# Optimization experiments

Measured on AMD Instinct MI355X. Metric: run time of the kernel, lower is better.

The kernel has to match this reference:

```python
import jax, jax.numpy as jnp
import numpy as np

N = 60000      # nodes
E = 240000     # edges
H = 256        # hidden_channels
M = 64         # middle_channels
F1 = 12        # num_radial * num_spherical**2
F2 = 6         # num_radial * num_spherical
L = 4          # num_layers (InterBlocks)
NL = 3         # num_output_layers (residual linears per block)
G = 2000       # number of graphs in batch
EPS = 1e-5


def setup_inputs() -> dict:
    key = jax.random.key(0)
    ks = iter(jax.random.split(key, 64))
    def nrm(shape, scale=0.05):
        return jax.random.normal(next(ks), shape, jnp.float32) * scale
    inp = {
        'x_idx': jax.random.randint(next(ks), (N, 9), 0, 178, jnp.int32),
        'edge_attr_idx': jax.random.randint(next(ks), (E, 3), 0, 18, jnp.int32),
        'edge_index': jax.random.randint(next(ks), (2, E), 0, N, jnp.int32),
        'batch': jnp.sort(jax.random.randint(next(ks), (N,), 0, G, jnp.int32)),
        'feature1': jax.random.uniform(next(ks), (E, F1), jnp.float32),
        'feature2': jax.random.uniform(next(ks), (E, F2), jnp.float32),
        # embeddings
        'x_tab': nrm((178, H)), 'e_tab': nrm((18, H)),
        # lin_x: Linear + BN + ReLU
        'linx_w': nrm((L, H, H)), 'linx_b': jnp.zeros((L, H)), 'linx_g': jnp.ones((L, H)), 'linx_be': jnp.zeros((L, H)),
        # lin_feat1: Linear(F1,M) + BN(M) + ReLU + Linear(M,H) + ReLU
        'f1_w1': nrm((L, F1, M)), 'f1_b1': jnp.zeros((L, M)), 'f1_g': jnp.ones((L, M)), 'f1_be': jnp.zeros((L, M)),
        'f1_w2': nrm((L, M, H)), 'f1_b2': jnp.zeros((L, H)),
        # lin_feat2: Linear(F2,M) + BN(M) + ReLU + Linear(M,H) + ReLU
        'f2_w1': nrm((L, F2, M)), 'f2_b1': jnp.zeros((L, M)), 'f2_g': jnp.ones((L, M)), 'f2_be': jnp.zeros((L, M)),
        'f2_w2': nrm((L, M, H)), 'f2_b2': jnp.zeros((L, H)),
        # EdgeGraphConv 1 & 2 (PyG GraphConv: lin_rel(aggr) + lin_root(x), root has no bias)
        'c1_rel_w': nrm((L, H, H)), 'c1_rel_b': jnp.zeros((L, H)), 'c1_root_w': nrm((L, H, H)),
        'c2_rel_w': nrm((L, H, H)), 'c2_rel_b': jnp.zeros((L, H)), 'c2_root_w': nrm((L, H, H)),
        # lin_cat
        'cat_w': nrm((L, 2 * H, H)), 'cat_b': jnp.zeros((L, H)),
        # residual linears
        'lins_w': nrm((L, NL, H, H)), 'lins_b': jnp.zeros((L, NL, H)),
        # GraphNorm
        'gn_w': jnp.ones((L, H)), 'gn_b': jnp.zeros((L, H)), 'gn_ms': jnp.ones((L, H)),
        # final
        'fin_w': nrm((L, H, H)), 'fin_b': jnp.zeros((L, H)),
    }
    return inp


def _bn(h, g, b):
    m = h.mean(0)
    v = jnp.mean((h - m) ** 2, axis=0)
    return (h - m) * jax.lax.rsqrt(v + EPS) * g + b


def _conv(x, src, dst, ew, rel_w, rel_b, root_w):
    # EdgeGraphConv: message = x_j * edge_weight, sum-aggregate at dst
    msg = x[src] * ew                                   # [E, H]
    agg = jax.ops.segment_sum(msg, dst, num_segments=N)  # [N, H]
    return agg @ rel_w + rel_b + x @ root_w


def _graphnorm(h, batch, w, b, ms):
    cnt = jnp.maximum(jax.ops.segment_sum(jnp.ones((h.shape[0], 1), h.dtype), batch, num_segments=G), 1.0)
    mean = jax.ops.segment_sum(h, batch, num_segments=G) / cnt
    out = h - ms * mean[batch]
    var = jax.ops.segment_sum(out ** 2, batch, num_segments=G) / cnt
    return out * jax.lax.rsqrt(var[batch] + EPS) * w + b


def reference(x_idx, edge_attr_idx, edge_index, batch, feature1, feature2, x_tab, e_tab,
              linx_w, linx_b, linx_g, linx_be,
              f1_w1, f1_b1, f1_g, f1_be, f1_w2, f1_b2,
              f2_w1, f2_b1, f2_g, f2_be, f2_w2, f2_b2,
              c1_rel_w, c1_rel_b, c1_root_w, c2_rel_w, c2_rel_b, c2_root_w,
              cat_w, cat_b, lins_w, lins_b, gn_w, gn_b, gn_ms, fin_w, fin_b):
    relu = jax.nn.relu
    x = x_tab[x_idx].sum(1)                 # [N, H] atom-feature embedding sum
    _e = e_tab[edge_attr_idx].sum(1)        # edge embedding (computed, unused downstream as in source)
    src, dst = edge_index[0], edge_index[1]
    for l in range(L):
        xl = relu(_bn(x @ linx_w[l] + linx_b[l], linx_g[l], linx_be[l]))
        w1 = relu(relu(_bn(feature1 @ f1_w1[l] + f1_b1[l], f1_g[l], f1_be[l])) @ f1_w2[l] + f1_b2[l])
        w2 = relu(relu(_bn(feature2 @ f2_w1[l] + f2_b1[l], f2_g[l], f2_be[l])) @ f2_w2[l] + f2_b2[l])
        h1 = relu(_conv(xl, src, dst, w1, c1_rel_w[l], c1_rel_b[l], c1_root_w[l]))
        h2 = relu(_conv(xl, src, dst, w2, c2_rel_w[l], c2_rel_b[l], c2_root_w[l]))
        h = relu(jnp.concatenate([h1, h2], axis=1) @ cat_w[l] + cat_b[l])
        h = h + xl
        for k in range(NL):
            h = relu(h @ lins_w[l, k] + lins_b[l, k]) + h
        h = _graphnorm(h, batch, gn_w[l], gn_b[l], gn_ms[l])
        x = h @ fin_w[l] + fin_b[l]
    return x
```

## Files before the change

### kernel.cpp

```cpp
#include <hip/hip_runtime.h>
#include <cstdint>

constexpr int Nn = 60000;
constexpr int Ee = 240000;
constexpr int Hh = 256;
constexpr int Mm = 64;
constexpr int F1c = 12;
constexpr int Lc = 4;
constexpr int NLc = 3;
constexpr int Gc = 2000;
constexpr float EPSc = 1e-5f;
constexpr int NB = (Nn + 255) / 256;
constexpr int CSB = 256;

typedef _Float16 f16x8 __attribute__((ext_vector_type(8)));
typedef __attribute__((ext_vector_type(4))) float f32x4;
typedef __attribute__((ext_vector_type(4))) unsigned short u16x4;
typedef unsigned short ushortt;

__device__ __forceinline__ ushortt f2h(float f) {
    union { _Float16 h; ushortt u; } c; c.h = (_Float16)f; return c.u;
}
__device__ __forceinline__ float h2f(ushortt u) {
    union { _Float16 h; ushortt u; } c; c.u = u; return (float)c.h;
}

__global__ void embed_x_kernel(const int* __restrict__ xidx, const float* __restrict__ xtab,
                               ushortt* __restrict__ x) {
    int n = blockIdx.x;
    int c = threadIdx.x;
    __shared__ int idx[9];
    if (c < 9) idx[c] = xidx[n * 9 + c];
    __syncthreads();
    float s = 0.f;
#pragma unroll
    for (int j = 0; j < 9; j++) s += xtab[idx[j] * Hh + c];
    x[(size_t)n * Hh + c] = f2h(s);
}

__global__ void seg_bounds_kernel(const int* __restrict__ batch, int* __restrict__ gstart) {
    int g = blockIdx.x * 256 + threadIdx.x;
    if (g > Gc) return;
    if (g == Gc) { gstart[Gc] = Nn; return; }
    int lo = 0, hi = Nn;
    while (lo < hi) { int mid = (lo + hi) >> 1; if (batch[mid] < g) lo = mid + 1; else hi = mid; }
    gstart[g] = lo;
}

__global__ void deg_hist_kernel(const int* __restrict__ ei, int* __restrict__ deg) {
    int e = blockIdx.x * 256 + threadIdx.x;
    if (e >= Ee) return;
    atomicAdd(&deg[ei[Ee + e]], 1);
}

__global__ void psum_block_kernel(const int* __restrict__ deg, int* __restrict__ iscan,
                                  int* __restrict__ bsum) {
    __shared__ int s[256];
    int t = threadIdx.x;
    int i = blockIdx.x * 256 + t;
    int v = (i < Nn) ? deg[i] : 0;
    s[t] = v;
    __syncthreads();
    for (int off = 1; off < 256; off <<= 1) {
        int add = (t >= off) ? s[t - off] : 0;
        __syncthreads();
        s[t] += add;
        __syncthreads();
    }
    if (i < Nn) iscan[i] = s[t];
    if (t == 255) bsum[blockIdx.x] = s[255];
}

__global__ void scan_bsum_kernel(const int* __restrict__ bsum, int* __restrict__ ebase,
                                 int* __restrict__ rowptr) {
    if (threadIdx.x != 0 || blockIdx.x != 0) return;
    int run = 0;
    for (int b = 0; b < NB; b++) { ebase[b] = run; run += bsum[b]; }
    rowptr[Nn] = Ee;
}

__global__ void finalize_rowptr_kernel(const int* __restrict__ deg, const int* __restrict__ iscan,
                                       const int* __restrict__ ebase, int* __restrict__ rowptr) {
    int i = blockIdx.x * 256 + threadIdx.x;
    if (i >= Nn) return;
    rowptr[i] = ebase[i >> 8] + iscan[i] - deg[i];
}

__global__ void fill_eid_kernel(const int* __restrict__ ei, int* __restrict__ cursor,
                                int* __restrict__ eid, int* __restrict__ esrc) {
    int e = blockIdx.x * 256 + threadIdx.x;
    if (e >= Ee) return;
    int dst = ei[Ee + e];
    int pos = atomicAdd(&cursor[dst], 1);
    eid[pos] = e;
    esrc[pos] = ei[e];
}

template<int K>
__global__ void gather_feat_kernel(const float* __restrict__ F, const int* __restrict__ eid,
                                   ushortt* __restrict__ featS) {
    long i = (long)blockIdx.x * 256 + threadIdx.x;
    if (i >= (long)Ee * K) return;
    int e = (int)(i / K);
    int k = (int)(i % K);
    featS[i] = f2h(F[(size_t)eid[e] * K + k]);
}

__global__ void wconv_kernel(const float* __restrict__ src, ushortt* __restrict__ dst,
                             int nmat, int K, long dstMS, int kOff, long srcMS) {
    long idx = (long)blockIdx.x * 256 + threadIdx.x;
    long tot = (long)nmat * 256 * K;
    if (idx >= tot) return;
    int k = (int)(idx % K);
    long t = idx / K;
    int c = (int)(t & 255);
    int m = (int)(t >> 8);
    float w = src[m * srcMS + (long)k * 256 + c];
    int kg = kOff + k;
    int ks = kg >> 5;
    int k5 = kg & 31;
    int kpp = (((k5 & 15) >> 2) << 3) + (((k5 >> 4) & 1) << 2) + (k5 & 3);
    long o = m * dstMS + ((long)ks * 256 + c) * 32 + kpp;
    dst[o] = f2h(w);
}

template<int K>
__global__ void gram_kernel(const float* __restrict__ F, float* __restrict__ G,
                            float* __restrict__ s) {
    constexpr int NP = K * (K + 1) / 2;
    __shared__ float Ft[256 * K];
    int tid = threadIdx.x;
    int pi = 0, pj = 0;
    if (tid < NP) {
        int tt = tid;
        for (pi = 0; pi < K; pi++) { if (tt <= pi) { pj = tt; break; } tt -= (pi + 1); }
    }
    float acc = 0.f;
    int ntiles = (Ee + 255) / 256;
    for (int tile = blockIdx.x; tile < ntiles; tile += gridDim.x) {
        long r0 = (long)tile * 256;
        for (int idx = tid; idx < 256 * K; idx += 256) {
            long r = r0 + idx / K;
            Ft[idx] = (r < Ee) ? F[r * K + idx % K] : 0.f;
        }
        __syncthreads();
        if (tid < NP) {
            for (int r = 0; r < 256; r++) acc += Ft[r * K + pi] * Ft[r * K + pj];
        } else if (tid < NP + K) {
            int i = tid - NP;
            for (int r = 0; r < 256; r++) acc += Ft[r * K + i];
        }
        __syncthreads();
    }
    if (tid < NP) {
        atomicAdd(&G[pi * K + pj], acc);
        if (pi != pj) atomicAdd(&G[pj * K + pi], acc);
    } else if (tid < NP + K) {
        atomicAdd(&s[tid - NP], acc);
    }
}

__global__ void gram_stats_kernel(const float* __restrict__ G, const float* __restrict__ s,
                                  const float* __restrict__ W, const float* __restrict__ b,
                                  int K, float Ecnt, float* __restrict__ colsum,
                                  float* __restrict__ colsq) {
    int m = threadIdx.x;
    float wm[F1c];
    for (int i = 0; i < K; i++) wm[i] = W[i * Mm + m];
    float sw = 0.f;
    for (int i = 0; i < K; i++) sw += s[i] * wm[i];
    float q = 0.f;
    for (int i = 0; i < K; i++) {
        float gi = 0.f;
        for (int j = 0; j < K; j++) gi += G[i * K + j] * wm[j];
        q += wm[i] * gi;
    }
    colsum[m] = sw + Ecnt * b[m];
    colsq[m] = q + 2.f * b[m] * sw + Ecnt * b[m] * b[m];
}

__global__ void colstats_part_kernel(const ushortt* __restrict__ A, long tot4,
                                     float* __restrict__ part) {
    __shared__ float ls[1024], lq[1024];
    int tid = threadIdx.x;
    long i0 = (long)blockIdx.x * 256 + tid;
    long stride = (long)gridDim.x * 256;
    float s[4] = {0, 0, 0, 0}, q[4] = {0, 0, 0, 0};
    for (long i = i0; i < tot4; i += stride) {
        u16x4 v = *(const u16x4*)(A + i * 4);
#pragma unroll
        for (int j = 0; j < 4; j++) { float f = h2f(v[j]); s[j] += f; q[j] += f * f; }
    }
#pragma unroll
    for (int j = 0; j < 4; j++) { ls[tid * 4 + j] = s[j]; lq[tid * 4 + j] = q[j]; }
    __syncthreads();
    if (tid < 64) {
#pragma unroll
        for (int j = 0; j < 4; j++) {
            float ts = ls[tid * 4 + j] + ls[(tid + 64) * 4 + j] +
                       ls[(tid + 128) * 4 + j] + ls[(tid + 192) * 4 + j];
            float tq = lq[tid * 4 + j] + lq[(tid + 64) * 4 + j] +
                       lq[(tid + 128) * 4 + j] + lq[(tid + 192) * 4 + j];
            part[(size_t)blockIdx.x * 512 + tid * 4 + j] = ts;
            part[(size_t)blockIdx.x * 512 + 256 + tid * 4 + j] = tq;
        }
    }
}

__global__ void colstats_reduce_kernel(const float* __restrict__ part,
                                       float* __restrict__ colsum, float* __restrict__ colsq) {
    int t = blockIdx.x * 256 + threadIdx.x;
    float acc = 0.f;
    for (int b = 0; b < CSB; b++) acc += part[(size_t)b * 512 + t];
    if (t < 256) colsum[t] = acc;
    else colsq[t - 256] = acc;
}

__global__ void bn_relu_h_kernel(const ushortt* __restrict__ A, ushortt* __restrict__ outp,
                                 const float* __restrict__ sum, const float* __restrict__ sq,
                                 const float* __restrict__ g, const float* __restrict__ be,
                                 float rinv, long tot4) {
    long i = (long)blockIdx.x * 256 + threadIdx.x;
    if (i >= tot4) return;
    int c0 = (int)((i * 4) & 255);
    u16x4 v = *(const u16x4*)(A + i * 4);
    u16x4 o;
#pragma unroll
    for (int j = 0; j < 4; j++) {
        int c = c0 + j;
        float m = sum[c] * rinv;
        float var = sq[c] * rinv - m * m;
        float f = (h2f(v[j]) - m) * rsqrtf(var + EPSc) * g[c] + be[c];
        o[j] = f2h(fmaxf(f, 0.f));
    }
    *(u16x4*)(outp + i * 4) = o;
}

__global__ void f2h_kernel(const float* __restrict__ src, ushortt* __restrict__ dst, long tot4) {
    long i = (long)blockIdx.x * 256 + threadIdx.x;
    if (i >= tot4) return;
    float4 v = *(const float4*)(src + i * 4);
    u16x4 o;
    o[0] = f2h(v.x); o[1] = f2h(v.y); o[2] = f2h(v.z); o[3] = f2h(v.w);
    *(u16x4*)(dst + i * 4) = o;
}

__global__ __launch_bounds__(256, 4) void bgemm_kernel(
    const ushortt* __restrict__ A1, int lda1, const ushortt* __restrict__ A2, int lda2,
    const ushortt* __restrict__ Wt,
    const float* __restrict__ bias, const ushortt* __restrict__ res,
    float* __restrict__ Cf, ushortt* __restrict__ Ch,
    int rows, int K1, int Ktot, int do_relu) {
    __shared__ char As[128 * 80];
    int tid = threadIdx.x;
    int lane = tid & 63;
    int wave = tid >> 6;
    int wrow0 = (wave >> 1) * 64;
    int wcol0 = (wave & 1) * 64;
    int r0 = blockIdx.y * 128;
    int j0 = blockIdx.x * 128;
    int l15 = lane & 15;
    int l4 = lane >> 4;

    f32x4 acc[4][4];
#pragma unroll
    for (int i = 0; i < 4; i++)
#pragma unroll
        for (int j = 0; j < 4; j++) acc[i][j] = (f32x4){0.f, 0.f, 0.f, 0.f};

    for (int kt = 0; kt < Ktot; kt += 32) {
        const ushortt* A; int lda; int koff;
        if (kt < K1) { A = A1; lda = lda1; koff = kt; }
        else         { A = A2; lda = lda2; koff = kt - K1; }
        f16x8 bh[4];
        long kb = ((long)(kt >> 5) * 256) * 32;
#pragma unroll
        for (int j = 0; j < 4; j++) {
            int colrow = j0 + wcol0 + j * 16 + l15;
            bh[j] = *(const f16x8*)(Wt + kb + (long)colrow * 32 + l4 * 8);
        }
#pragma unroll
        for (int p = 0; p < 4; p++) {
            int fid = p * 256 + tid;
            int row = fid >> 3;
            int k4 = (fid & 7) * 4;
            int rg = r0 + row; if (rg >= rows) rg = rows - 1;
            u16x4 hv = *(const u16x4*)(A + (size_t)rg * lda + koff + k4);
            int off = (((k4 & 15) >> 2) << 4) + ((k4 >> 4) << 3);
            *(u16x4*)(As + row * 80 + off) = hv;
        }
        __syncthreads();

        f16x8 ah[4];
#pragma unroll
        for (int i = 0; i < 4; i++) {
            int row = wrow0 + i * 16 + l15;
            ah[i] = *(const f16x8*)(As + row * 80 + l4 * 16);
        }
#pragma unroll
        for (int i = 0; i < 4; i++)
#pragma unroll
            for (int j = 0; j < 4; j++)
                acc[i][j] = __builtin_amdgcn_mfma_f32_16x16x32_f16(ah[i], bh[j], acc[i][j], 0, 0, 0);
        __syncthreads();
    }

#pragma unroll
    for (int i = 0; i < 4; i++) {
#pragma unroll
        for (int r = 0; r < 4; r++) {
            int row = r0 + wrow0 + i * 16 + l4 * 4 + r;
            if (row >= rows) continue;
#pragma unroll
            for (int j = 0; j < 4; j++) {
                int col = j0 + wcol0 + j * 16 + l15;
                float v = acc[i][j][r] + bias[col];
                if (do_relu) v = fmaxf(v, 0.f);
                if (res) v += h2f(res[(size_t)row * 256 + col]);
                if (Cf) Cf[(size_t)row * 256 + col] = v;
                if (Ch) Ch[(size_t)row * 256 + col] = f2h(v);
            }
        }
    }
}

template<int K>
__global__ __launch_bounds__(256, 4) void edge_gemm_kernel(
    const ushortt* __restrict__ featS, const float* __restrict__ W1,
    const float* __restrict__ b1,
    const float* __restrict__ colsum, const float* __restrict__ colsq,
    const float* __restrict__ g, const float* __restrict__ be, float rinv,
    const ushortt* __restrict__ Wt, const float* __restrict__ bias,
    ushortt* __restrict__ Wc, int c0, int ec) {
    __shared__ char As[2][128 * 80];
    __shared__ float Fs[128 * K];
    __shared__ float W1s[K * 64];
    __shared__ float b1s[64], scs[64], shs[64];
    int tid = threadIdx.x;
    for (int i = tid; i < K * 64; i += 256) W1s[i] = W1[i];
    if (tid < 64) {
        float mu = colsum[tid] * rinv;
        float var = colsq[tid] * rinv - mu * mu;
        float rs = rsqrtf(var + EPSc) * g[tid];
        scs[tid] = rs;
        shs[tid] = be[tid] - mu * rs;
        b1s[tid] = b1[tid];
    }
    int r0 = blockIdx.y * 128;
    for (int idx = tid; idx < 128 * K; idx += 256) {
        int row = idx / K;
        long e = (long)c0 + r0 + row;
        if (e >= Ee) e = Ee - 1;
        Fs[idx] = h2f(featS[e * K + idx % K]);
    }
    __syncthreads();
    {
        int row = tid >> 1;
        int m0 = (tid & 1) * 32;
        const float* fr = &Fs[row * K];
#pragma unroll
        for (int mm = 0; mm < 32; mm++) {
            int m = m0 + mm;
            float u = b1s[m];
#pragma unroll
            for (int k = 0; k < K; k++) u += fr[k] * W1s[k * 64 + m];
            float v = fmaxf(u * scs[m] + shs[m], 0.f);
            int k5 = m & 31;
            int kpp = (((k5 & 15) >> 2) << 3) + (((k5 >> 4) & 1) << 2) + (k5 & 3);
            *(ushortt*)(As[m >> 5] + row * 80 + kpp * 2) = f2h(v);
        }
    }
    __syncthreads();

    int lane = tid & 63;
    int wave = tid >> 6;
    int wrow0 = (wave >> 1) * 64;
    int wcol0 = (wave & 1) * 64;
    int j0 = blockIdx.x * 128;
    int l15 = lane & 15;
    int l4 = lane >> 4;

    f32x4 acc[4][4];
#pragma unroll
    for (int i = 0; i < 4; i++)
#pragma unroll
        for (int j = 0; j < 4; j++) acc[i][j] = (f32x4){0.f, 0.f, 0.f, 0.f};

#pragma unroll
    for (int kt = 0; kt < 64; kt += 32) {
        f16x8 bh[4];
        long kb = ((long)(kt >> 5) * 256) * 32;
#pragma unroll
        for (int j = 0; j < 4; j++) {
            int colrow = j0 + wcol0 + j * 16 + l15;
            bh[j] = *(const f16x8*)(Wt + kb + (long)colrow * 32 + l4 * 8);
        }
        f16x8 ah[4];
        const char* Az = As[kt >> 5];
#pragma unroll
        for (int i = 0; i < 4; i++) {
            int row = wrow0 + i * 16 + l15;
            ah[i] = *(const f16x8*)(Az + row * 80 + l4 * 16);
        }
#pragma unroll
        for (int i = 0; i < 4; i++)
#pragma unroll
            for (int j = 0; j < 4; j++)
                acc[i][j] = __builtin_amdgcn_mfma_f32_16x16x32_f16(ah[i], bh[j], acc[i][j], 0, 0, 0);
    }

#pragma unroll
    for (int i = 0; i < 4; i++) {
#pragma unroll
        for (int r = 0; r < 4; r++) {
            int row = wrow0 + i * 16 + l4 * 4 + r;
            if (r0 + row >= ec) continue;
#pragma unroll
            for (int j = 0; j < 4; j++) {
                int col = j0 + wcol0 + j * 16 + l15;
                float v = fmaxf(acc[i][j][r] + bias[col], 0.f);
                Wc[(size_t)(r0 + row) * 256 + col] = f2h(v);
            }
        }
    }
}

__global__ __launch_bounds__(256) void gather_agg_kernel(
    const int* __restrict__ rowptr, const int* __restrict__ esrc,
    const ushortt* __restrict__ Wc, const ushortt* __restrict__ xl,
    float* __restrict__ agg, int c0, int c1, int first) {
    int n = (blockIdx.x * 256 + threadIdx.x) >> 6;
    if (n >= Nn) return;
    int lane = threadIdx.x & 63;
    int rs = rowptr[n], re = rowptr[n + 1];
    if (rs < c0) rs = c0;
    if (re > c1) re = c1;
    float* ap = agg + (size_t)n * Hh + lane * 4;
    float4 acc;
    if (first) {
        acc = make_float4(0.f, 0.f, 0.f, 0.f);
    } else {
        if (rs >= re) return;
        acc = *(float4*)ap;
    }
    for (int i = rs; i < re; i++) {
        u16x4 wv = *(const u16x4*)(Wc + (size_t)(i - c0) * Hh + lane * 4);
        u16x4 xv = *(const u16x4*)(xl + (size_t)esrc[i] * Hh + lane * 4);
        acc.x += h2f(wv[0]) * h2f(xv[0]);
        acc.y += h2f(wv[1]) * h2f(xv[1]);
        acc.z += h2f(wv[2]) * h2f(xv[2]);
        acc.w += h2f(wv[3]) * h2f(xv[3]);
    }
    *(float4*)ap = acc;
}

__global__ void gn_mean_h_kernel(const ushortt* __restrict__ h, const int* __restrict__ gstart,
                                 float* __restrict__ mean) {
    int g = blockIdx.x, c = threadIdx.x;
    int s = gstart[g], e = gstart[g + 1];
    float acc = 0.f;
    for (int n = s; n < e; n++) acc += h2f(h[(size_t)n * Hh + c]);
    float cnt = (float)((e - s) > 1 ? (e - s) : 1);
    mean[(size_t)g * Hh + c] = acc / cnt;
}

__global__ void gn_out_h_kernel(const ushortt* __restrict__ h, const float* __restrict__ mean,
                                const int* __restrict__ batch, const float* __restrict__ ms,
                                ushortt* __restrict__ outp) {
    long i = (long)blockIdx.x * 256 + threadIdx.x;
    if (i >= (long)Nn * Hh / 4) return;
    int n = (int)((i * 4) >> 8);
    int c0 = (int)((i * 4) & 255);
    const float* mrow = mean + (size_t)batch[n] * Hh;
    u16x4 v = *(const u16x4*)(h + i * 4);
    u16x4 o;
#pragma unroll
    for (int j = 0; j < 4; j++) o[j] = f2h(h2f(v[j]) - ms[c0 + j] * mrow[c0 + j]);
    *(u16x4*)(outp + i * 4) = o;
}

__global__ void gn_rstd_h_kernel(const ushortt* __restrict__ outp, const int* __restrict__ gstart,
                                 float* __restrict__ rstd) {
    int g = blockIdx.x, c = threadIdx.x;
    int s = gstart[g], e = gstart[g + 1];
    float acc = 0.f;
    for (int n = s; n < e; n++) { float v = h2f(outp[(size_t)n * Hh + c]); acc += v * v; }
    float cnt = (float)((e - s) > 1 ? (e - s) : 1);
    rstd[(size_t)g * Hh + c] = rsqrtf(acc / cnt + EPSc);
}

__global__ void gn_apply_h_kernel(ushortt* __restrict__ outp, const float* __restrict__ rstd,
                                  const int* __restrict__ batch, const float* __restrict__ w,
                                  const float* __restrict__ b) {
    long i = (long)blockIdx.x * 256 + threadIdx.x;
    if (i >= (long)Nn * Hh / 4) return;
    int n = (int)((i * 4) >> 8);
    int c0 = (int)((i * 4) & 255);
    const float* rrow = rstd + (size_t)batch[n] * Hh;
    u16x4 v = *(const u16x4*)(outp + i * 4);
    u16x4 o;
#pragma unroll
    for (int j = 0; j < 4; j++)
        o[j] = f2h(h2f(v[j]) * rrow[c0 + j] * w[c0 + j] + b[c0 + j]);
    *(u16x4*)(outp + i * 4) = o;
}

extern "C" void kernel_launch(void* const* d_in, const int* in_sizes, int n_in,
                              void* d_out, int out_size, void* d_ws, size_t ws_size,
                              hipStream_t stream) {
    const int* x_idx      = (const int*)d_in[0];
    const int* edge_index = (const int*)d_in[2];
    const int* batch      = (const int*)d_in[3];
    const float* feature1 = (const float*)d_in[4];
    const float* feature2 = (const float*)d_in[5];
    const float* x_tab    = (const float*)d_in[6];
    const float* linx_w   = (const float*)d_in[8];
    const float* linx_b   = (const float*)d_in[9];
    const float* linx_g   = (const float*)d_in[10];
    const float* linx_be  = (const float*)d_in[11];
    const float* f1_w1    = (const float*)d_in[12];
    const float* f1_b1    = (const float*)d_in[13];
    const float* f1_g     = (const float*)d_in[14];
    const float* f1_be    = (const float*)d_in[15];
    const float* f1_w2    = (const float*)d_in[16];
    const float* f1_b2    = (const float*)d_in[17];
    const float* f2_w1    = (const float*)d_in[18];
    const float* f2_b1    = (const float*)d_in[19];
    const float* f2_g     = (const float*)d_in[20];
    const float* f2_be    = (const float*)d_in[21];
    const float* f2_w2    = (const float*)d_in[22];
    const float* f2_b2    = (const float*)d_in[23];
    const float* c1_rel_w  = (const float*)d_in[24];
    const float* c1_rel_b  = (const float*)d_in[25];
    const float* c1_root_w = (const float*)d_in[26];
    const float* c2_rel_w  = (const float*)d_in[27];
    const float* c2_rel_b  = (const float*)d_in[28];
    const float* c2_root_w = (const float*)d_in[29];
    const float* cat_w    = (const float*)d_in[30];
    const float* cat_b    = (const float*)d_in[31];
    const float* lins_w   = (const float*)d_in[32];
    const float* lins_b   = (const float*)d_in[33];
    const float* gn_w     = (const float*)d_in[34];
    const float* gn_b     = (const float*)d_in[35];
    const float* gn_ms    = (const float*)d_in[36];
    const float* fin_w    = (const float*)d_in[37];
    const float* fin_b    = (const float*)d_in[38];

    size_t NH = (size_t)Nn * Hh;
    char* p = (char*)d_ws;
    ushortt* X  = (ushortt*)p; p += NH * 2;
    ushortt* B1 = (ushortt*)p; p += NH * 2;
    ushortt* B2 = (ushortt*)p; p += NH * 2;
    ushortt* B3 = (ushortt*)p; p += NH * 2;
    ushortt* B4 = (ushortt*)p; p += NH * 2;
    float* aggF = (float*)d_out;
    float* gmean = (float*)p; p += (size_t)Gc * Hh * 4;
    float* grstd = (float*)p; p += (size_t)Gc * Hh * 4;
    float* colsum = (float*)p; p += 256 * 4;
    float* colsq  = (float*)p; p += 256 * 4;
    float* part = (float*)p; p += (size_t)CSB * 512 * 4;
    float* G1 = (float*)p; p += 160 * 4;
    float* s1 = (float*)p; p += 16 * 4;
    float* G2 = (float*)p; p += 48 * 4;
    float* s2 = (float*)p; p += 16 * 4;
    int* gstart = (int*)p; p += 2048 * 4;
    int* deg    = (int*)p; p += Nn * 4;
    int* iscan  = (int*)p; p += Nn * 4;
    int* rowptr = (int*)p; p += (Nn + 256) * 4;
    int* cursor = (int*)p; p += Nn * 4;
    int* bsum   = (int*)p; p += 256 * 4;
    int* ebase  = (int*)p; p += 256 * 4;
    int* eid    = (int*)p; p += (size_t)Ee * 4;
    int* esrc   = (int*)p; p += (size_t)Ee * 4;
    ushortt* featS1 = (ushortt*)p; p += (size_t)Ee * F1c * 2;
    ushortt* featS2 = (ushortt*)p; p += (size_t)Ee * 6 * 2;
    ushortt* linxW = (ushortt*)p; p += (size_t)4 * 65536 * 2;
    ushortt* convW = (ushortt*)p; p += (size_t)16 * 65536 * 2;
    ushortt* catW  = (ushortt*)p; p += (size_t)8 * 65536 * 2;
    ushortt* linsW = (ushortt*)p; p += (size_t)12 * 65536 * 2;
    ushortt* finW  = (ushortt*)p; p += (size_t)4 * 65536 * 2;
    ushortt* fw2W  = (ushortt*)p; p += (size_t)8 * 16384 * 2;
    long availB = (long)ws_size - (long)(p - (char*)d_ws) - 1024;
    int CE = (int)(availB / (Hh * 2));
    if (CE > Ee) CE = Ee;
    if (CE < 8000) CE = 8000;
    ushortt* Wcb = (ushortt*)p;

    long tot4 = (long)NH / 4;
    int blks4 = (int)((tot4 + 255) / 256);
    int blksE = (Ee + 255) / 256;
    int blksN = (Nn + 255) / 256;

    embed_x_kernel<<<Nn, 256, 0, stream>>>(x_idx, x_tab, X);
    seg_bounds_kernel<<<(Gc + 256) / 256, 256, 0, stream>>>(batch, gstart);
    hipMemsetAsync(deg, 0, Nn * sizeof(int), stream);
    deg_hist_kernel<<<blksE, 256, 0, stream>>>(edge_index, deg);
    psum_block_kernel<<<NB, 256, 0, stream>>>(deg, iscan, bsum);
    scan_bsum_kernel<<<1, 64, 0, stream>>>(bsum, ebase, rowptr);
    finalize_rowptr_kernel<<<blksN, 256, 0, stream>>>(deg, iscan, ebase, rowptr);
    hipMemcpyAsync(cursor, rowptr, Nn * sizeof(int), hipMemcpyDeviceToDevice, stream);
    fill_eid_kernel<<<blksE, 256, 0, stream>>>(edge_index, cursor, eid, esrc);
    gather_feat_kernel<F1c><<<(int)(((long)Ee * F1c + 255) / 256), 256, 0, stream>>>(
        feature1, eid, featS1);
    gather_feat_kernel<6><<<(int)(((long)Ee * 6 + 255) / 256), 256, 0, stream>>>(
        feature2, eid, featS2);

    hipMemsetAsync(G1, 0, 240 * sizeof(float), stream);
    gram_kernel<F1c><<<240, 256, 0, stream>>>(feature1, G1, s1);
    gram_kernel<6><<<240, 256, 0, stream>>>(feature2, G2, s2);

    auto wcv = [&](const float* src, ushortt* dh, int nmat, int K,
                   long dstMS, int kOff, long srcMS) {
        long tot = (long)nmat * 256 * K;
        wconv_kernel<<<(int)((tot + 255) / 256), 256, 0, stream>>>(src, dh, nmat, K,
                                                                   dstMS, kOff, srcMS);
    };
    wcv(linx_w, linxW, 4, 256, 65536, 0, 65536);
    wcv(c1_rel_w,  convW,          4, 256, 262144, 0,   65536);
    wcv(c1_root_w, convW,          4, 256, 262144, 256, 65536);
    wcv(c2_rel_w,  convW + 131072, 4, 256, 262144, 0,   65536);
    wcv(c2_root_w, convW + 131072, 4, 256, 262144, 256, 65536);
    wcv(cat_w, catW, 4, 512, 131072, 0, 131072);
    wcv(lins_w, linsW, 12, 256, 65536, 0, 65536);
    wcv(fin_w, finW, 4, 256, 65536, 0, 65536);
    wcv(f1_w2, fw2W,         4, 64, 32768, 0, 16384);
    wcv(f2_w2, fw2W + 16384, 4, 64, 32768, 0, 16384);

    dim3 gN(2, (Nn + 127) / 128);

    for (int l = 0; l < Lc; l++) {
        bgemm_kernel<<<gN, 256, 0, stream>>>(X, 256, nullptr, 0,
                                             linxW + (size_t)l * 65536,
                                             linx_b + l * Hh, nullptr, nullptr, B1,
                                             Nn, 256, 256, 0);
        colstats_part_kernel<<<CSB, 256, 0, stream>>>(B1, tot4, part);
        colstats_reduce_kernel<<<2, 256, 0, stream>>>(part, colsum, colsq);
        bn_relu_h_kernel<<<blks4, 256, 0, stream>>>(B1, X, colsum, colsq,
                                                    linx_g + l * Hh, linx_be + l * Hh,
                                                    1.f / Nn, tot4);

        for (int br = 0; br < 2; br++) {
            const float* fw1 = br == 0 ? f1_w1 + (size_t)l * F1c * Mm : f2_w1 + (size_t)l * 6 * Mm;
            const float* fb1 = br == 0 ? f1_b1 + l * Mm : f2_b1 + l * Mm;
            const float* fg  = br == 0 ? f1_g + l * Mm  : f2_g + l * Mm;
            const float* fbe = br == 0 ? f1_be + l * Mm : f2_be + l * Mm;
            const float* fb2 = br == 0 ? f1_b2 + l * Hh : f2_b2 + l * Hh;
            const float* Gg = br == 0 ? G1 : G2;
            const float* sg = br == 0 ? s1 : s2;
            const float* relb = br == 0 ? c1_rel_b + l * Hh : c2_rel_b + l * Hh;
            int Kf = br == 0 ? F1c : 6;
            ushortt* fw2t = fw2W + (size_t)l * 32768 + (br ? 16384 : 0);
            ushortt* cvt  = convW + (size_t)l * 262144 + (br ? 131072 : 0);
            ushortt* hbr = br == 0 ? B3 : B2;

            gram_stats_kernel<<<1, 64, 0, stream>>>(Gg, sg, fw1, fb1, Kf, (float)Ee,
                                                    colsum, colsq);
            for (int c0 = 0; c0 < Ee; c0 += CE) {
                int ec = Ee - c0 < CE ? Ee - c0 : CE;
                dim3 gc(2, (ec + 127) / 128);
                if (br == 0)
                    edge_gemm_kernel<F1c><<<gc, 256, 0, stream>>>(
                        featS1, fw1, fb1, colsum, colsq, fg, fbe, 1.f / Ee,
                        fw2t, fb2, Wcb, c0, ec);
                else
                    edge_gemm_kernel<6><<<gc, 256, 0, stream>>>(
                        featS2, fw1, fb1, colsum, colsq, fg, fbe, 1.f / Ee,
                        fw2t, fb2, Wcb, c0, ec);
                gather_agg_kernel<<<(Nn * 64 + 255) / 256, 256, 0, stream>>>(
                    rowptr, esrc, Wcb, X, aggF, c0, c0 + ec, c0 == 0 ? 1 : 0);
            }
            f2h_kernel<<<blks4, 256, 0, stream>>>(aggF, B4, tot4);
            bgemm_kernel<<<gN, 256, 0, stream>>>(B4, 256, X, 256, cvt,
                                                 relb, nullptr, nullptr, hbr,
                                                 Nn, 256, 512, 1);
        }

        bgemm_kernel<<<gN, 256, 0, stream>>>(B3, 256, B2, 256,
                                             catW + (size_t)l * 131072,
                                             cat_b + l * Hh, X, nullptr, B1,
                                             Nn, 256, 512, 1);
        ushortt* cur = B1; ushortt* oth = B2;
        for (int k = 0; k < NLc; k++) {
            bgemm_kernel<<<gN, 256, 0, stream>>>(cur, 256, nullptr, 0,
                                                 linsW + ((size_t)l * NLc + k) * 65536,
                                                 lins_b + ((size_t)l * NLc + k) * Hh, cur,
                                                 nullptr, oth, Nn, 256, 256, 1);
            ushortt* t = cur; cur = oth; oth = t;
        }
        gn_mean_h_kernel<<<Gc, 256, 0, stream>>>(cur, gstart, gmean);
        gn_out_h_kernel<<<blks4, 256, 0, stream>>>(cur, gmean, batch, gn_ms + l * Hh, oth);
        gn_rstd_h_kernel<<<Gc, 256, 0, stream>>>(oth, gstart, grstd);
        gn_apply_h_kernel<<<blks4, 256, 0, stream>>>(oth, grstd, batch, gn_w + l * Hh,
                                                     gn_b + l * Hh);
        bgemm_kernel<<<gN, 256, 0, stream>>>(oth, 256, nullptr, 0,
                                             finW + (size_t)l * 65536,
                                             fin_b + l * Hh, nullptr,
                                             (l == Lc - 1) ? (float*)d_out : nullptr,
                                             (l == Lc - 1) ? nullptr : X,
                                             Nn, 256, 256, 0);
    }
}
```

Before: 3.262 ms.

## Prefetch next K-tile in bgemm and fuse fp32-to-fp16 conversion into GEMM loads

The GEMM main loop now register-prefetches the next A tile and weight fragments while MFMAs run on the current tile, so global load latency overlaps with compute. The conv GEMM also reads the fp32 aggregation buffer directly and converts it to fp16 while loading, which removes the separate f2h kernel and the B4 workspace round trip. The cost is extra registers for the prefetch buffers, which may lower occupancy under launch_bounds(256,4), and a runtime branch on the A element type.

```diff
diff --git a/kernel.cpp b/kernel.cpp
--- a/kernel.cpp
+++ b/kernel.cpp
@@ -236,21 +236,12 @@
     *(u16x4*)(outp + i * 4) = o;
 }
 
-__global__ void f2h_kernel(const float* __restrict__ src, ushortt* __restrict__ dst, long tot4) {
-    long i = (long)blockIdx.x * 256 + threadIdx.x;
-    if (i >= tot4) return;
-    float4 v = *(const float4*)(src + i * 4);
-    u16x4 o;
-    o[0] = f2h(v.x); o[1] = f2h(v.y); o[2] = f2h(v.z); o[3] = f2h(v.w);
-    *(u16x4*)(dst + i * 4) = o;
-}
-
 __global__ __launch_bounds__(256, 4) void bgemm_kernel(
-    const ushortt* __restrict__ A1, int lda1, const ushortt* __restrict__ A2, int lda2,
+    const void* __restrict__ A1v, int lda1, const ushortt* __restrict__ A2, int lda2,
     const ushortt* __restrict__ Wt,
     const float* __restrict__ bias, const ushortt* __restrict__ res,
     float* __restrict__ Cf, ushortt* __restrict__ Ch,
-    int rows, int K1, int Ktot, int do_relu) {
+    int rows, int K1, int Ktot, int do_relu, int a1f32) {
     __shared__ char As[128 * 80];
     int tid = threadIdx.x;
     int lane = tid & 63;
@@ -262,35 +253,63 @@
     int l15 = lane & 15;
     int l4 = lane >> 4;
 
-    f32x4 acc[4][4];
-#pragma unroll
-    for (int i = 0; i < 4; i++)
-#pragma unroll
-        for (int j = 0; j < 4; j++) acc[i][j] = (f32x4){0.f, 0.f, 0.f, 0.f};
-
-    for (int kt = 0; kt < Ktot; kt += 32) {
-        const ushortt* A; int lda; int koff;
-        if (kt < K1) { A = A1; lda = lda1; koff = kt; }
-        else         { A = A2; lda = lda2; koff = kt - K1; }
-        f16x8 bh[4];
+    int srow[4], sk4[4], soff[4];
+#pragma unroll
+    for (int p = 0; p < 4; p++) {
+        int fid = p * 256 + tid;
+        srow[p] = fid >> 3;
+        sk4[p] = (fid & 7) * 4;
+        soff[p] = srow[p] * 80 + ((((sk4[p] & 15) >> 2) << 4) + ((sk4[p] >> 4) << 3));
+    }
+
+    auto loadA = [&](int kt, u16x4* hv) {
+        const void* Av; int lda; int koff; int f32;
+        if (kt < K1) { Av = A1v; lda = lda1; koff = kt; f32 = a1f32; }
+        else         { Av = (const void*)A2; lda = lda2; koff = kt - K1; f32 = 0; }
+#pragma unroll
+        for (int p = 0; p < 4; p++) {
+            int rg = r0 + srow[p]; if (rg >= rows) rg = rows - 1;
+            if (f32) {
+                float4 v = *(const float4*)((const float*)Av + (size_t)rg * lda + koff + sk4[p]);
+                u16x4 h;
+                h[0] = f2h(v.x); h[1] = f2h(v.y); h[2] = f2h(v.z); h[3] = f2h(v.w);
+                hv[p] = h;
+            } else {
+                hv[p] = *(const u16x4*)((const ushortt*)Av + (size_t)rg * lda + koff + sk4[p]);
+            }
+        }
+    };
+    auto loadW = [&](int kt, f16x8* bh) {
         long kb = ((long)(kt >> 5) * 256) * 32;
 #pragma unroll
         for (int j = 0; j < 4; j++) {
             int colrow = j0 + wcol0 + j * 16 + l15;
             bh[j] = *(const f16x8*)(Wt + kb + (long)colrow * 32 + l4 * 8);
         }
-#pragma unroll
-        for (int p = 0; p < 4; p++) {
-            int fid = p * 256 + tid;
-            int row = fid >> 3;
-            int k4 = (fid & 7) * 4;
-            int rg = r0 + row; if (rg >= rows) rg = rows - 1;
-            u16x4 hv = *(const u16x4*)(A + (size_t)rg * lda + koff + k4);
-            int off = (((k4 & 15) >> 2) << 4) + ((k4 >> 4) << 3);
-            *(u16x4*)(As + row * 80 + off) = hv;
-        }
-        __syncthreads();
-
+    };
+
+    f32x4 acc[4][4];
+#pragma unroll
+    for (int i = 0; i < 4; i++)
+#pragma unroll
+        for (int j = 0; j < 4; j++) acc[i][j] = (f32x4){0.f, 0.f, 0.f, 0.f};
+
+    int nst = Ktot >> 5;
+    u16x4 hv[4];
+    f16x8 bhc[4], bhn[4];
+    loadA(0, hv);
+    loadW(0, bhc);
+#pragma unroll
+    for (int p = 0; p < 4; p++) *(u16x4*)(As + soff[p]) = hv[p];
+    __syncthreads();
+
+    for (int st = 0; st < nst; st++) {
+        bool more = (st + 1 < nst);
+        u16x4 hn[4];
+        if (more) {
+            loadA((st + 1) << 5, hn);
+            loadW((st + 1) << 5, bhn);
+        }
         f16x8 ah[4];
 #pragma unroll
         for (int i = 0; i < 4; i++) {
@@ -301,8 +320,15 @@
         for (int i = 0; i < 4; i++)
 #pragma unroll
             for (int j = 0; j < 4; j++)
-                acc[i][j] = __builtin_amdgcn_mfma_f32_16x16x32_f16(ah[i], bh[j], acc[i][j], 0, 0, 0);
-        __syncthreads();
+                acc[i][j] = __builtin_amdgcn_mfma_f32_16x16x32_f16(ah[i], bhc[j], acc[i][j], 0, 0, 0);
+        if (more) {
+            __syncthreads();
+#pragma unroll
+            for (int p = 0; p < 4; p++) *(u16x4*)(As + soff[p]) = hn[p];
+            __syncthreads();
+#pragma unroll
+            for (int j = 0; j < 4; j++) bhc[j] = bhn[j];
+        }
     }
 
 #pragma unroll
@@ -552,7 +578,6 @@
     ushortt* B1 = (ushortt*)p; p += NH * 2;
     ushortt* B2 = (ushortt*)p; p += NH * 2;
     ushortt* B3 = (ushortt*)p; p += NH * 2;
-    ushortt* B4 = (ushortt*)p; p += NH * 2;
     float* aggF = (float*)d_out;
     float* gmean = (float*)p; p += (size_t)Gc * Hh * 4;
     float* grstd = (float*)p; p += (size_t)Gc * Hh * 4;
@@ -632,7 +657,7 @@
         bgemm_kernel<<<gN, 256, 0, stream>>>(X, 256, nullptr, 0,
                                              linxW + (size_t)l * 65536,
                                              linx_b + l * Hh, nullptr, nullptr, B1,
-                                             Nn, 256, 256, 0);
+                                             Nn, 256, 256, 0, 0);
         colstats_part_kernel<<<CSB, 256, 0, stream>>>(B1, tot4, part);
         colstats_reduce_kernel<<<2, 256, 0, stream>>>(part, colsum, colsq);
         bn_relu_h_kernel<<<blks4, 256, 0, stream>>>(B1, X, colsum, colsq,
@@ -669,22 +694,21 @@
                 gather_agg_kernel<<<(Nn * 64 + 255) / 256, 256, 0, stream>>>(
                     rowptr, esrc, Wcb, X, aggF, c0, c0 + ec, c0 == 0 ? 1 : 0);
             }
-            f2h_kernel<<<blks4, 256, 0, stream>>>(aggF, B4, tot4);
-            bgemm_kernel<<<gN, 256, 0, stream>>>(B4, 256, X, 256, cvt,
+            bgemm_kernel<<<gN, 256, 0, stream>>>(aggF, 256, X, 256, cvt,
                                                  relb, nullptr, nullptr, hbr,
-                                                 Nn, 256, 512, 1);
+                                                 Nn, 256, 512, 1, 1);
         }
 
         bgemm_kernel<<<gN, 256, 0, stream>>>(B3, 256, B2, 256,
                                              catW + (size_t)l * 131072,
                                              cat_b + l * Hh, X, nullptr, B1,
-                                             Nn, 256, 512, 1);
+                                             Nn, 256, 512, 1, 0);
         ushortt* cur = B1; ushortt* oth = B2;
         for (int k = 0; k < NLc; k++) {
             bgemm_kernel<<<gN, 256, 0, stream>>>(cur, 256, nullptr, 0,
                                                  linsW + ((size_t)l * NLc + k) * 65536,
                                                  lins_b + ((size_t)l * NLc + k) * Hh, cur,
-                                                 nullptr, oth, Nn, 256, 256, 1);
+                                                 nullptr, oth, Nn, 256, 256, 1, 0);
             ushortt* t = cur; cur = oth; oth = t;
         }
         gn_mean_h_kernel<<<Gc, 256, 0, stream>>>(cur, gstart, gmean);
@@ -697,6 +721,6 @@
                                              fin_b + l * Hh, nullptr,
                                              (l == Lc - 1) ? (float*)d_out : nullptr,
                                              (l == Lc - 1) ? nullptr : X,
-                                             Nn, 256, 256, 0);
-    }
-}
+                                             Nn, 256, 256, 0, 0);
+    }
+}
```

Measured after the change: 3.321 ms. Within noise of the previous version (+1.8%).
